# Optimization experiments

Measured on AMD Instinct MI355X. Metric: run time of the kernel, lower is better.

## Reference

```python
import jax, jax.numpy as jnp
import numpy as np

B, S, E = 4, 2048, 1024

def setup_inputs() -> dict:
    key = jax.random.key(0)
    ks = jax.random.split(key, 9)
    lim = 1.0 / np.sqrt(E)
    inp = {
        "query": jax.random.normal(ks[0], (B, S, E), dtype=jnp.float32),
        "key": jax.random.normal(ks[1], (B, S, E), dtype=jnp.float32),
        "value": jax.random.normal(ks[2], (B, S, E), dtype=jnp.float32),
        "Wq": jax.random.uniform(ks[3], (E, E), jnp.float32, -lim, lim),
        "bq": jax.random.uniform(ks[4], (E,), jnp.float32, -lim, lim),
        "Wk": jax.random.uniform(ks[5], (E, E), jnp.float32, -lim, lim),
        "bk": jax.random.uniform(ks[6], (E,), jnp.float32, -lim, lim),
        "Wv": jax.random.uniform(ks[7], (E, E), jnp.float32, -lim, lim),
        "bv": jax.random.uniform(ks[8], (E,), jnp.float32, -lim, lim),
    }
    return inp

def reference(query, key, value, Wq, bq, Wk, bk, Wv, bv):
    # Linear layers (torch stores weight as [out,in]; here W is [in,out] used as x @ W)
    q = query @ Wq + bq            # [B,S,E]
    k = key @ Wk + bk              # [B,S,E]
    v = value @ Wv + bv            # [B,S,E]
    inv_scale = jnp.asarray(E, q.dtype) ** 0.5
    scores = jnp.einsum("bse,bte->bst", q, k) / inv_scale  # [B,S,S]
    attn = jax.nn.softmax(scores, axis=-1)
    # dropout_p = 0.0 -> identity
    out = jnp.einsum("bst,bte->bse", attn, v)  # [B,S,E]
    return out
```

## Files before the change

kernel.cpp:

```cpp
#include <hip/hip_runtime.h>
#include <hip/hip_bf16.h>


typedef __bf16 bf16_t;
typedef bf16_t bf16x8 __attribute__((ext_vector_type(8)));
typedef bf16_t bf16x4 __attribute__((ext_vector_type(4)));
typedef float  f32x4  __attribute__((ext_vector_type(4)));

typedef const __attribute__((address_space(1))) unsigned gl_uint;
typedef __attribute__((address_space(3))) unsigned lds_uint;

#define BM 128
#define BN 128
#define BK 64

__device__ __forceinline__ void gload_lds16(const void* g, void* l) {
  __builtin_amdgcn_global_load_lds((gl_uint*)g, (lds_uint*)l, 16, 0, 0);
}

#define VMCNT(N) asm volatile("s_waitcnt vmcnt(" #N ")" ::: "memory")
#define LGKM0()  asm volatile("s_waitcnt lgkmcnt(0)" ::: "memory")

template <int KS, int NT, bool LSUM>
__device__ __forceinline__ void gemm_v3(
    const bf16_t* __restrict__ Ab, const bf16_t* __restrict__ Bb,
    bf16_t* Lb, f32x4 acc[4][4], f32x4 acc_l[4])
{
  const int tid  = threadIdx.x;
  const int lane = tid & 63;
  const int l15  = lane & 15;
  const int quad = lane >> 4;
  const int wid  = tid >> 6;
  const int wr   = wid >> 1;
  const int wcl  = wid & 1;
  const int swz0 = (quad ^ (l15 & 7)) * 8;
  const int swz1 = ((quad + 4) ^ (l15 & 7)) * 8;

  bf16x8 ones;
#pragma unroll
  for (int t = 0; t < 8; ++t) ones[t] = (bf16_t)1.0f;

  const int r8 = tid >> 3, s8 = tid & 7;
  const size_t gbase = (size_t)r8 * KS + (size_t)((s8 ^ (r8 & 7)) * 8);
  const int dbase = tid * 8;

#define SLOTA(s) (Lb + (s) * 24576)
#define SLOTB(s) (Lb + (s) * 24576 + 16384)
#define STAGE6(ktile, slot) { \
    const bf16_t* _A = Ab + (size_t)(ktile) * 64; \
    const bf16_t* _B = Bb + (size_t)(ktile) * 64; \
    bf16_t* _la = SLOTA(slot); bf16_t* _lb = SLOTB(slot); \
    gload_lds16(_A + gbase,                      _la + dbase); \
    gload_lds16(_A + gbase + (size_t)64 * KS,    _la + dbase + 4096); \
    gload_lds16(_A + gbase + (size_t)128 * KS,   _la + dbase + 8192); \
    gload_lds16(_A + gbase + (size_t)192 * KS,   _la + dbase + 12288); \
    gload_lds16(_B + gbase,                      _lb + dbase); \
    gload_lds16(_B + gbase + (size_t)64 * KS,    _lb + dbase + 4096); }

  const int aoff = (wr * 64 + l15) * 64;
  const int boff = (wcl * 64 + l15) * 64;

#define RD(slot, FA, FB) { \
    const bf16_t* _a = SLOTA(slot) + aoff; \
    const bf16_t* _b = SLOTB(slot) + boff; \
    _Pragma("unroll") for (int mi = 0; mi < 4; ++mi) { \
      FA[mi][0] = *(const bf16x8*)(_a + mi * 1024 + swz0); \
      FA[mi][1] = *(const bf16x8*)(_a + mi * 1024 + swz1); } \
    _Pragma("unroll") for (int ni = 0; ni < 4; ++ni) { \
      FB[ni][0] = *(const bf16x8*)(_b + ni * 1024 + swz0); \
      FB[ni][1] = *(const bf16x8*)(_b + ni * 1024 + swz1); } }

#define MFM(FA, FB) { \
    _Pragma("unroll") for (int kk = 0; kk < 2; ++kk) { \
      _Pragma("unroll") for (int mi = 0; mi < 4; ++mi) \
      _Pragma("unroll") for (int ni = 0; ni < 4; ++ni) \
        acc[mi][ni] = __builtin_amdgcn_mfma_f32_16x16x32_bf16( \
            FA[mi][kk], FB[ni][kk], acc[mi][ni], 0, 0, 0); \
      if constexpr (LSUM) { \
        _Pragma("unroll") for (int mi = 0; mi < 4; ++mi) \
          acc_l[mi] = __builtin_amdgcn_mfma_f32_16x16x32_bf16( \
              FA[mi][kk], ones, acc_l[mi], 0, 0, 0); } } }

  bf16x8 fa0[4][2], fb0[4][2], fa1[4][2], fb1[4][2];

  STAGE6(0, 0); STAGE6(1, 1); STAGE6(2, 2);
  VMCNT(6);
  __builtin_amdgcn_s_barrier();
  RD(0, fa0, fb0);
  LGKM0();
  __builtin_amdgcn_s_barrier();

#pragma unroll
  for (int kt = 0; kt < NT - 2; ++kt) {
    const int ss = kt % 3;
    const int rs = (kt + 1) % 3;
    if (kt <= NT - 4) STAGE6(kt + 3, ss);
    if ((kt & 1) == 0) { RD(rs, fa1, fb1); MFM(fa0, fb0); }
    else               { RD(rs, fa0, fb0); MFM(fa1, fb1); }
    if (kt <= NT - 4) { VMCNT(6); }
    else              { VMCNT(0); }
    __builtin_amdgcn_s_barrier();
  }
  RD((NT - 1) % 3, fa1, fb1); MFM(fa0, fb0);
  MFM(fa1, fb1);

#undef SLOTA
#undef SLOTB
#undef STAGE6
#undef RD
#undef MFM
}

__device__ __forceinline__ void mfma_tile128(const bf16_t* As, const bf16_t* Bs,
                                             f32x4 acc[4][4]) {
  const int lane = threadIdx.x & 63;
  const int quad = lane >> 4;
  const int l15  = lane & 15;
  const int wid  = threadIdx.x >> 6;
  const int wm   = (wid >> 1) * 64;
  const int wn   = (wid & 1) * 64;
  const int csw  = l15 & 7;
#pragma unroll
  for (int ks = 0; ks < 2; ++ks) {
    const int sg = ks * 4 + quad;
    const int c  = (sg ^ csw) * 8;
    bf16x8 fa[4], fb[4];
#pragma unroll
    for (int i = 0; i < 4; ++i)
      fa[i] = *(const bf16x8*)&As[(wm + i * 16 + l15) * BK + c];
#pragma unroll
    for (int i = 0; i < 4; ++i)
      fb[i] = *(const bf16x8*)&Bs[(wn + i * 16 + l15) * BK + c];
#pragma unroll
    for (int mi = 0; mi < 4; ++mi)
#pragma unroll
      for (int ni = 0; ni < 4; ++ni)
        acc[mi][ni] = __builtin_amdgcn_mfma_f32_16x16x32_bf16(
            fa[mi], fb[ni], acc[mi][ni], 0, 0, 0);
  }
}

__device__ __forceinline__ void gemm_core128(
    const bf16_t* __restrict__ Ab, const bf16_t* __restrict__ Bb,
    const int K, bf16_t* As, bf16_t* Bs, f32x4 acc[4][4])
{
  const int tid = threadIdx.x;
  for (int kt = 0; kt < K; kt += BK) {
#pragma unroll
    for (int j = 0; j < 4; ++j) {
      const int lin = j * 256 + tid;
      const int row = lin >> 3;
      const int seg = (lin & 7) ^ (row & 7);
      gload_lds16(Ab + (size_t)row * K + kt + seg * 8, &As[lin * 8]);
    }
#pragma unroll
    for (int j = 0; j < 4; ++j) {
      const int lin = j * 256 + tid;
      const int row = lin >> 3;
      const int seg = (lin & 7) ^ (row & 7);
      gload_lds16(Bb + (size_t)row * K + kt + seg * 8, &Bs[lin * 8]);
    }
    __syncthreads();
    mfma_tile128(As, Bs, acc);
    __syncthreads();
  }
}

__global__ __launch_bounds__(256, 2)
void qkv_proj(const bf16_t* __restrict__ qb, const bf16_t* __restrict__ kb,
              const bf16_t* __restrict__ vb, const bf16_t* __restrict__ Wqt,
              const bf16_t* __restrict__ Wkt, const bf16_t* __restrict__ Wvt,
              const float* __restrict__ bq, const float* __restrict__ bk,
              const float* __restrict__ bv, bf16_t* __restrict__ qp,
              bf16_t* __restrict__ kp, bf16_t* __restrict__ vT)
{
  __shared__ __align__(16) bf16_t As[BM * BK];
  __shared__ __align__(16) bf16_t Bs[BN * BK];

  const int L = blockIdx.x;
  const int g = L >> 3;
  const int gst = (L & 7) * 3 + (g >> 6);
  const int z  = gst >> 3;
  const int sy = gst & 7;
  const int w  = g & 63;
  const int bx = w & 7;
  const int by = sy * 8 + (w >> 3);

  const bf16_t* A    = (z == 0) ? qb : (z == 1) ? kb : vb;
  const bf16_t* W    = (z == 0) ? Wqt : (z == 1) ? Wkt : Wvt;
  const float*  bias = (z == 0) ? bq : (z == 1) ? bk : bv;
  const int K = 1024, N = 1024;
  const bf16_t* Ab = A + (size_t)by * BM * K;
  const bf16_t* Bb = W + (size_t)bx * BN * K;

  f32x4 acc[4][4];
  const f32x4 z4 = {0.f, 0.f, 0.f, 0.f};
#pragma unroll
  for (int i = 0; i < 4; ++i)
#pragma unroll
    for (int j = 0; j < 4; ++j) acc[i][j] = z4;

  gemm_core128(Ab, Bb, K, As, Bs, acc);

  const int lane = threadIdx.x & 63;
  const int quad = lane >> 4;
  const int l15  = lane & 15;
  const int wid  = threadIdx.x >> 6;
  const int wm = (wid >> 1) * 64, wn = (wid & 1) * 64;
  const int m0 = by * BM, n0 = bx * BN;
#pragma unroll
  for (int mi = 0; mi < 4; ++mi) {
#pragma unroll
    for (int ni = 0; ni < 4; ++ni) {
      const int gn = n0 + wn + ni * 16 + l15;
      const int gm = m0 + wm + mi * 16 + quad * 4;
      const float bv_ = bias[gn];
      f32x4 a = acc[mi][ni];
      if (z < 2) {
        bf16_t* C = (z == 0) ? qp : kp;
#pragma unroll
        for (int r = 0; r < 4; ++r)
          C[(size_t)(gm + r) * N + gn] = (bf16_t)(a[r] + bv_);
      } else {
        const int b = gm >> 11;
        const int s = gm & 2047;
        bf16x4 o;
#pragma unroll
        for (int r = 0; r < 4; ++r) o[r] = (bf16_t)(a[r] + bv_);
        *(bf16x4*)&vT[((size_t)b * N + gn) * 2048 + s] = o;
      }
    }
  }
}

__global__ __launch_bounds__(512, 2)
void scores_v3(const bf16_t* __restrict__ qp, const bf16_t* __restrict__ kp,
               bf16_t* __restrict__ P)
{
  __shared__ __align__(16) bf16_t lds[3 * 24576];
  const int L   = blockIdx.x;
  const int lin = (L & 7) * 64 + (L >> 3);
  const int bz  = lin >> 7;
  const int r   = lin & 127;
  const int by  = r >> 4, bx = r & 15;
  const int K = 1024;

  const bf16_t* Ab = qp + (size_t)bz * 2048 * 1024 + (size_t)by * 256 * K;
  const bf16_t* Bb = kp + (size_t)bz * 2048 * 1024 + (size_t)bx * 128 * K;

  f32x4 acc[4][4];
  f32x4 acc_l[4];
  const f32x4 z4 = {0.f, 0.f, 0.f, 0.f};
#pragma unroll
  for (int i = 0; i < 4; ++i) {
    acc_l[i] = z4;
#pragma unroll
    for (int j = 0; j < 4; ++j) acc[i][j] = z4;
  }

  gemm_v3<1024, 16, false>(Ab, Bb, lds, acc, acc_l);

  const int tid = threadIdx.x;
  const int lane = tid & 63, l15 = lane & 15, quad = lane >> 4;
  const int wid = tid >> 6, wr = wid >> 1, wcl = wid & 1;
  const int m0 = by * 256 + wr * 64;
  const int n0 = bx * 128 + wcl * 64;
  bf16_t* C = P + (size_t)bz * 2048 * 2048;
  const float cexp = 0.03125f * 1.4426950408889634f;
#pragma unroll
  for (int mi = 0; mi < 4; ++mi) {
    const int gm = m0 + mi * 16 + quad * 4;
#pragma unroll
    for (int ni = 0; ni < 4; ++ni) {
      const int gn = n0 + ni * 16 + l15;
      f32x4 a = acc[mi][ni];
#pragma unroll
      for (int rr = 0; rr < 4; ++rr)
        C[(size_t)(gm + rr) * 2048 + gn] = (bf16_t)exp2f(a[rr] * cexp);
    }
  }
}

__global__ __launch_bounds__(512, 2)
void pv_v3(const bf16_t* __restrict__ P, const bf16_t* __restrict__ vT,
           float* __restrict__ out)
{
  __shared__ __align__(16) bf16_t lds[3 * 24576];
  const int L   = blockIdx.x;
  const int lin = (L & 7) * 32 + (L >> 3);
  const int bz  = lin >> 6;
  const int r   = lin & 63;
  const int by  = r >> 3, bx = r & 7;

  const bf16_t* Ab = P  + (size_t)bz * 2048 * 2048 + (size_t)by * 256 * 2048;
  const bf16_t* Bb = vT + (size_t)bz * 1024 * 2048 + (size_t)bx * 128 * 2048;

  f32x4 acc[4][4];
  f32x4 acc_l[4];
  const f32x4 z4 = {0.f, 0.f, 0.f, 0.f};
#pragma unroll
  for (int i = 0; i < 4; ++i) {
    acc_l[i] = z4;
#pragma unroll
    for (int j = 0; j < 4; ++j) acc[i][j] = z4;
  }

  gemm_v3<2048, 32, true>(Ab, Bb, lds, acc, acc_l);

  const int tid = threadIdx.x;
  const int lane = tid & 63, l15 = lane & 15, quad = lane >> 4;
  const int wid = tid >> 6, wr = wid >> 1, wcl = wid & 1;
  const int m0 = by * 256 + wr * 64;
  const int n0 = bx * 128 + wcl * 64;
  float* C = out + (size_t)bz * 2048 * 1024;
#pragma unroll
  for (int mi = 0; mi < 4; ++mi) {
    const int gm = m0 + mi * 16 + quad * 4;
    float il[4];
#pragma unroll
    for (int rr = 0; rr < 4; ++rr) il[rr] = 1.0f / acc_l[mi][rr];
#pragma unroll
    for (int ni = 0; ni < 4; ++ni) {
      const int gn = n0 + ni * 16 + l15;
      f32x4 a = acc[mi][ni];
#pragma unroll
      for (int rr = 0; rr < 4; ++rr)
        C[(size_t)(gm + rr) * 1024 + gn] = a[rr] * il[rr];
    }
  }
}

__global__ __launch_bounds__(256)
void prep(const float* __restrict__ q, const float* __restrict__ k,
          const float* __restrict__ v, const float* __restrict__ Wq,
          const float* __restrict__ Wk, const float* __restrict__ Wv,
          bf16_t* __restrict__ qo, bf16_t* __restrict__ ko,
          bf16_t* __restrict__ vo, bf16_t* __restrict__ Wqt,
          bf16_t* __restrict__ Wkt, bf16_t* __restrict__ Wvt) {
  const int L = blockIdx.x;
  const int tid = threadIdx.x;
  if (L < 24576) {
    const int z = L >> 13;
    const int blk = L & 8191;
    const float* in = (z == 0) ? q : (z == 1) ? k : v;
    bf16_t* out = (z == 0) ? qo : (z == 1) ? ko : vo;
    const size_t i = ((size_t)blk * 256 + tid) * 4;
    const float4 w = *(const float4*)(in + i);
    bf16x4 o;
    o[0] = (bf16_t)w.x; o[1] = (bf16_t)w.y; o[2] = (bf16_t)w.z; o[3] = (bf16_t)w.w;
    *(bf16x4*)(out + i) = o;
  } else {
    const int t = L - 24576;
    const int z = t >> 8;
    const int wi = t & 255;
    const float* W = (z == 0) ? Wq : (z == 1) ? Wk : Wv;
    bf16_t* Wt = (z == 0) ? Wqt : (z == 1) ? Wkt : Wvt;
    __shared__ float tile[64][65];
    const int n0 = (wi & 15) * 64;
    const int k0 = (wi >> 4) * 64;
#pragma unroll
    for (int it = 0; it < 16; ++it) {
      const int idx = it * 256 + tid;
      const int r = idx >> 6, c = idx & 63;
      tile[r][c] = W[(size_t)(k0 + r) * 1024 + n0 + c];
    }
    __syncthreads();
#pragma unroll
    for (int it = 0; it < 16; ++it) {
      const int idx = it * 256 + tid;
      const int r = idx >> 6, c = idx & 63;
      Wt[(size_t)(n0 + r) * 1024 + k0 + c] = (bf16_t)tile[c][r];
    }
  }
}

extern "C" void kernel_launch(void* const* d_in, const int* in_sizes, int n_in,
                              void* d_out, int out_size, void* d_ws, size_t ws_size,
                              hipStream_t stream) {
  const int B = 4, S = 2048, E = 1024;
  const size_t BSE = (size_t)B * S * E;
  const size_t EE  = (size_t)E * E;

  const float* q_in = (const float*)d_in[0];
  const float* k_in = (const float*)d_in[1];
  const float* v_in = (const float*)d_in[2];
  const float* Wq = (const float*)d_in[3];
  const float* bq = (const float*)d_in[4];
  const float* Wk = (const float*)d_in[5];
  const float* bk = (const float*)d_in[6];
  const float* Wv = (const float*)d_in[7];
  const float* bv = (const float*)d_in[8];
  float* out = (float*)d_out;

  char* ws = (char*)d_ws;
  bf16_t* Wqt = (bf16_t*)ws;
  bf16_t* Wkt = Wqt + EE;
  bf16_t* Wvt = Wkt + EE;
  bf16_t* qb  = Wvt + EE;
  bf16_t* kb  = qb + BSE;
  bf16_t* vb  = kb + BSE;
  bf16_t* qp  = vb + BSE;
  bf16_t* kp  = qp + BSE;
  bf16_t* vT  = kp + BSE;
  bf16_t* P   = vT + BSE;

  prep<<<25344, 256, 0, stream>>>(q_in, k_in, v_in, Wq, Wk, Wv,
                                  qb, kb, vb, Wqt, Wkt, Wvt);

  qkv_proj<<<1536, 256, 0, stream>>>(qb, kb, vb, Wqt, Wkt, Wvt,
                                     bq, bk, bv, qp, kp, vT);

  scores_v3<<<512, 512, 0, stream>>>(qp, kp, P);

  pv_v3<<<256, 512, 0, stream>>>(P, vT, out);

  (void)in_sizes; (void)n_in; (void)out_size; (void)ws_size;
}
```

Baseline: 288.1 us.

## Compute softmax row sums in scores epilogue and use 128-tile PV kernel

Moves the softmax denominator computation out of the PV GEMM, where extra MFMAs against a ones vector accumulated row sums, into the scores epilogue. There the rounded bf16 exponentials are summed with wave shuffles and atomically added into a zeroed row-sum buffer. The PV stage switches to a 256-thread, 128x128 tile kernel (gemm_core128) with 512 blocks that divides by the precomputed sums. This drops a fifth of the PV MFMAs and doubles its block count. The cost is a memset, global float atomics and extra epilogue work in the scores kernel.

```diff
diff --git a/kernel.cpp b/kernel.cpp
--- a/kernel.cpp
+++ b/kernel.cpp
@@ -21,10 +21,10 @@
 #define VMCNT(N) asm volatile("s_waitcnt vmcnt(" #N ")" ::: "memory")
 #define LGKM0()  asm volatile("s_waitcnt lgkmcnt(0)" ::: "memory")
 
-template <int KS, int NT, bool LSUM>
+template <int KS, int NT>
 __device__ __forceinline__ void gemm_v3(
     const bf16_t* __restrict__ Ab, const bf16_t* __restrict__ Bb,
-    bf16_t* Lb, f32x4 acc[4][4], f32x4 acc_l[4])
+    bf16_t* Lb, f32x4 acc[4][4])
 {
   const int tid  = threadIdx.x;
   const int lane = tid & 63;
@@ -35,10 +35,6 @@
   const int wcl  = wid & 1;
   const int swz0 = (quad ^ (l15 & 7)) * 8;
   const int swz1 = ((quad + 4) ^ (l15 & 7)) * 8;
-
-  bf16x8 ones;
-#pragma unroll
-  for (int t = 0; t < 8; ++t) ones[t] = (bf16_t)1.0f;
 
   const int r8 = tid >> 3, s8 = tid & 7;
   const size_t gbase = (size_t)r8 * KS + (size_t)((s8 ^ (r8 & 7)) * 8);
@@ -70,16 +66,12 @@
       FB[ni][0] = *(const bf16x8*)(_b + ni * 1024 + swz0); \
       FB[ni][1] = *(const bf16x8*)(_b + ni * 1024 + swz1); } }
 
-#define MFM(FA, FB) { \
-    _Pragma("unroll") for (int kk = 0; kk < 2; ++kk) { \
-      _Pragma("unroll") for (int mi = 0; mi < 4; ++mi) \
-      _Pragma("unroll") for (int ni = 0; ni < 4; ++ni) \
-        acc[mi][ni] = __builtin_amdgcn_mfma_f32_16x16x32_bf16( \
-            FA[mi][kk], FB[ni][kk], acc[mi][ni], 0, 0, 0); \
-      if constexpr (LSUM) { \
-        _Pragma("unroll") for (int mi = 0; mi < 4; ++mi) \
-          acc_l[mi] = __builtin_amdgcn_mfma_f32_16x16x32_bf16( \
-              FA[mi][kk], ones, acc_l[mi], 0, 0, 0); } } }
+#define MFM(FA, FB) \
+    _Pragma("unroll") for (int kk = 0; kk < 2; ++kk) \
+    _Pragma("unroll") for (int mi = 0; mi < 4; ++mi) \
+    _Pragma("unroll") for (int ni = 0; ni < 4; ++ni) \
+      acc[mi][ni] = __builtin_amdgcn_mfma_f32_16x16x32_bf16( \
+          FA[mi][kk], FB[ni][kk], acc[mi][ni], 0, 0, 0);
 
   bf16x8 fa0[4][2], fb0[4][2], fa1[4][2], fb1[4][2];
 
@@ -235,7 +227,7 @@
 
 __global__ __launch_bounds__(512, 2)
 void scores_v3(const bf16_t* __restrict__ qp, const bf16_t* __restrict__ kp,
-               bf16_t* __restrict__ P)
+               bf16_t* __restrict__ P, float* __restrict__ lsum)
 {
   __shared__ __align__(16) bf16_t lds[3 * 24576];
   const int L   = blockIdx.x;
@@ -249,16 +241,13 @@
   const bf16_t* Bb = kp + (size_t)bz * 2048 * 1024 + (size_t)bx * 128 * K;
 
   f32x4 acc[4][4];
-  f32x4 acc_l[4];
   const f32x4 z4 = {0.f, 0.f, 0.f, 0.f};
 #pragma unroll
-  for (int i = 0; i < 4; ++i) {
-    acc_l[i] = z4;
+  for (int i = 0; i < 4; ++i)
 #pragma unroll
     for (int j = 0; j < 4; ++j) acc[i][j] = z4;
-  }
-
-  gemm_v3<1024, 16, false>(Ab, Bb, lds, acc, acc_l);
+
+  gemm_v3<1024, 16>(Ab, Bb, lds, acc);
 
   const int tid = threadIdx.x;
   const int lane = tid & 63, l15 = lane & 15, quad = lane >> 4;
@@ -266,66 +255,78 @@
   const int m0 = by * 256 + wr * 64;
   const int n0 = bx * 128 + wcl * 64;
   bf16_t* C = P + (size_t)bz * 2048 * 2048;
+  float* lsb = lsum + (size_t)bz * 2048;
   const float cexp = 0.03125f * 1.4426950408889634f;
 #pragma unroll
   for (int mi = 0; mi < 4; ++mi) {
     const int gm = m0 + mi * 16 + quad * 4;
 #pragma unroll
+    for (int rr = 0; rr < 4; ++rr) {
+      float rs = 0.f;
+#pragma unroll
+      for (int ni = 0; ni < 4; ++ni) {
+        const int gn = n0 + ni * 16 + l15;
+        const bf16_t ob = (bf16_t)exp2f(acc[mi][ni][rr] * cexp);
+        C[(size_t)(gm + rr) * 2048 + gn] = ob;
+        rs += (float)ob;
+      }
+      rs += __shfl_xor(rs, 1, 64);
+      rs += __shfl_xor(rs, 2, 64);
+      rs += __shfl_xor(rs, 4, 64);
+      rs += __shfl_xor(rs, 8, 64);
+      if (l15 == 0) atomicAdd(&lsb[gm + rr], rs);
+    }
+  }
+}
+
+__global__ __launch_bounds__(256, 2)
+void pv128(const bf16_t* __restrict__ P, const bf16_t* __restrict__ vT,
+           const float* __restrict__ lsum, float* __restrict__ out)
+{
+  __shared__ __align__(16) bf16_t As[BM * BK];
+  __shared__ __align__(16) bf16_t Bs[BN * BK];
+
+  const int L = blockIdx.x;
+  const int xcd = L & 7;
+  const int w = (L >> 3) & 63;
+  const int bz = xcd >> 1;
+  const int bx = w & 7;
+  const int by = (xcd & 1) * 8 + (w >> 3);
+
+  const bf16_t* Ab = P  + (size_t)bz * 2048 * 2048 + (size_t)by * BM * 2048;
+  const bf16_t* Bb = vT + (size_t)bz * 1024 * 2048 + (size_t)bx * BN * 2048;
+
+  f32x4 acc[4][4];
+  const f32x4 z4 = {0.f, 0.f, 0.f, 0.f};
+#pragma unroll
+  for (int i = 0; i < 4; ++i)
+#pragma unroll
+    for (int j = 0; j < 4; ++j) acc[i][j] = z4;
+
+  gemm_core128(Ab, Bb, 2048, As, Bs, acc);
+
+  const int lane = threadIdx.x & 63;
+  const int quad = lane >> 4;
+  const int l15  = lane & 15;
+  const int wid  = threadIdx.x >> 6;
+  const int wm = (wid >> 1) * 64, wn = (wid & 1) * 64;
+  const int m0 = by * BM, n0 = bx * BN;
+  const float* ls = lsum + (size_t)bz * 2048;
+  float* C = out + (size_t)bz * 2048 * 1024;
+#pragma unroll
+  for (int mi = 0; mi < 4; ++mi) {
+    const int gm = m0 + wm + mi * 16 + quad * 4;
+    const f32x4 lv = *(const f32x4*)&ls[gm];
+    float il[4];
+#pragma unroll
+    for (int r = 0; r < 4; ++r) il[r] = 1.0f / lv[r];
+#pragma unroll
     for (int ni = 0; ni < 4; ++ni) {
-      const int gn = n0 + ni * 16 + l15;
+      const int gn = n0 + wn + ni * 16 + l15;
       f32x4 a = acc[mi][ni];
 #pragma unroll
-      for (int rr = 0; rr < 4; ++rr)
-        C[(size_t)(gm + rr) * 2048 + gn] = (bf16_t)exp2f(a[rr] * cexp);
-    }
-  }
-}
-
-__global__ __launch_bounds__(512, 2)
-void pv_v3(const bf16_t* __restrict__ P, const bf16_t* __restrict__ vT,
-           float* __restrict__ out)
-{
-  __shared__ __align__(16) bf16_t lds[3 * 24576];
-  const int L   = blockIdx.x;
-  const int lin = (L & 7) * 32 + (L >> 3);
-  const int bz  = lin >> 6;
-  const int r   = lin & 63;
-  const int by  = r >> 3, bx = r & 7;
-
-  const bf16_t* Ab = P  + (size_t)bz * 2048 * 2048 + (size_t)by * 256 * 2048;
-  const bf16_t* Bb = vT + (size_t)bz * 1024 * 2048 + (size_t)bx * 128 * 2048;
-
-  f32x4 acc[4][4];
-  f32x4 acc_l[4];
-  const f32x4 z4 = {0.f, 0.f, 0.f, 0.f};
-#pragma unroll
-  for (int i = 0; i < 4; ++i) {
-    acc_l[i] = z4;
-#pragma unroll
-    for (int j = 0; j < 4; ++j) acc[i][j] = z4;
-  }
-
-  gemm_v3<2048, 32, true>(Ab, Bb, lds, acc, acc_l);
-
-  const int tid = threadIdx.x;
-  const int lane = tid & 63, l15 = lane & 15, quad = lane >> 4;
-  const int wid = tid >> 6, wr = wid >> 1, wcl = wid & 1;
-  const int m0 = by * 256 + wr * 64;
-  const int n0 = bx * 128 + wcl * 64;
-  float* C = out + (size_t)bz * 2048 * 1024;
-#pragma unroll
-  for (int mi = 0; mi < 4; ++mi) {
-    const int gm = m0 + mi * 16 + quad * 4;
-    float il[4];
-#pragma unroll
-    for (int rr = 0; rr < 4; ++rr) il[rr] = 1.0f / acc_l[mi][rr];
-#pragma unroll
-    for (int ni = 0; ni < 4; ++ni) {
-      const int gn = n0 + ni * 16 + l15;
-      f32x4 a = acc[mi][ni];
-#pragma unroll
-      for (int rr = 0; rr < 4; ++rr)
-        C[(size_t)(gm + rr) * 1024 + gn] = a[rr] * il[rr];
+      for (int r = 0; r < 4; ++r)
+        C[(size_t)(gm + r) * 1024 + gn] = a[r] * il[r];
     }
   }
 }
@@ -403,6 +404,7 @@
   bf16_t* kp  = qp + BSE;
   bf16_t* vT  = kp + BSE;
   bf16_t* P   = vT + BSE;
+  float* lsum = (float*)qb;
 
   prep<<<25344, 256, 0, stream>>>(q_in, k_in, v_in, Wq, Wk, Wv,
                                   qb, kb, vb, Wqt, Wkt, Wvt);
@@ -410,9 +412,11 @@
   qkv_proj<<<1536, 256, 0, stream>>>(qb, kb, vb, Wqt, Wkt, Wvt,
                                      bq, bk, bv, qp, kp, vT);
 
-  scores_v3<<<512, 512, 0, stream>>>(qp, kp, P);
-
-  pv_v3<<<256, 512, 0, stream>>>(P, vT, out);
+  hipMemsetAsync(lsum, 0, (size_t)B * S * sizeof(float), stream);
+
+  scores_v3<<<512, 512, 0, stream>>>(qp, kp, P, lsum);
+
+  pv128<<<512, 256, 0, stream>>>(P, vT, lsum, out);
 
   (void)in_sizes; (void)n_in; (void)out_size; (void)ws_size;
 }
```

After: 302.0 us. +4.8%, slower.
